# Optimization experiments

Hardware: AMD Instinct MI355X
Metric: run time of the kernel (lower is better)

Reference implementation:

```python
import jax, jax.numpy as jnp
import numpy as np
from jax import lax


def _l2n(t, eps=1e-12):
    n = jnp.sqrt(jnp.sum(t * t, axis=-1, keepdims=True))
    return t / jnp.maximum(n, eps)


def _ln(t, w, b, eps=1e-5):
    mu = jnp.mean(t, -1, keepdims=True)
    var = jnp.var(t, -1, keepdims=True)
    return (t - mu) / jnp.sqrt(var + eps) * w + b


def _unfold3(x):
    # nn.Unfold(kernel_size=3, padding=1, stride=1): [B,C,H,W] -> [B,C,9,H*W]
    B, C, H, W = x.shape
    xp = jnp.pad(x, ((0, 0), (0, 0), (1, 1), (1, 1)))
    pat = jnp.stack([xp[:, :, i:i + H, j:j + W] for i in range(3) for j in range(3)], axis=2)
    return pat.reshape(B, C, 9, H * W)


def _forward(x, norm1_w, norm1_b, q_w, q_b, kv_w, kv_b, temperature, query_embedding,
             learnable_tokens, learnable_bias, sr_w, sr_b, pln_w, pln_b, proj_w, proj_b,
             norm2_w, norm2_b, fc1_w, fc1_b, dw_w, dw_b, fc2_w, fc2_b):
    B, C, H, W = x.shape
    nh = temperature.shape[0]
    d = C // nh
    N = H * W
    K = 9  # local_len = window_size**2
    # norm1 (WithBias LayerNorm over channel dim, channels-last)
    y = _ln(x.reshape(B, C, N).transpose(0, 2, 1), norm1_w, norm1_b)  # [B,N,C]
    # ---- AggregatedAttention ----
    q = (y @ q_w.T + q_b).reshape(B, N, nh, d).transpose(0, 2, 1, 3)  # [B,h,N,d]
    qn = _l2n(q)
    qs = (qn + query_embedding) * jax.nn.softplus(temperature)
    kv = y @ kv_w.T + kv_b  # [B,N,2C]
    k_loc = _l2n(kv[..., :C].reshape(B, N, nh, d)).reshape(B, N, C)
    kvl = jnp.concatenate([k_loc, kv[..., C:]], -1).transpose(0, 2, 1).reshape(B, 2 * C, H, W)
    pat = _unfold3(kvl).reshape(B, 2 * nh, d, K, N).transpose(0, 1, 4, 2, 3)  # [B,2h,N,d,K]
    k_l, v_l = pat[:, :nh], pat[:, nh:]
    attn_local = jnp.einsum('bhnd,bhndk->bhnk', qs, k_l)  # [B,h,N,K]
    # pooled branch; sr_ratio=1 so adaptive_avg_pool2d is identity
    y4 = y.transpose(0, 2, 1).reshape(B, C, H, W)
    xp = jax.nn.gelu(jnp.einsum('oc,bchw->bohw', sr_w, y4) + sr_b[:, None, None], approximate=False)
    xp = _ln(xp.reshape(B, C, N).transpose(0, 2, 1), pln_w, pln_b)  # [B,pool_len,C]
    kvp = (xp @ kv_w.T + kv_b).reshape(B, N, 2 * nh, d).transpose(0, 2, 1, 3)
    k_p = _l2n(kvp[:, :nh])
    v_p = kvp[:, nh:]
    attn_pool = jnp.einsum('bhnd,bhmd->bhnm', qs, k_p)  # [B,h,N,pool_len]
    attn = jax.nn.softmax(jnp.concatenate([attn_local, attn_pool], -1), axis=-1)
    a_l, a_p = attn[..., :K], attn[..., K:]
    w_l = jnp.einsum('bhnd,hdk->bhnk', qn, learnable_tokens) + learnable_bias + a_l
    x_local = jnp.einsum('bhnk,bhndk->bhnd', w_l, v_l)
    x_pool = jnp.einsum('bhnm,bhmd->bhnd', a_p, v_p)
    xo = (x_local + x_pool).transpose(0, 2, 1, 3).reshape(B, N, C)
    # proj then raw torch-style reshape [B,N,C] -> [B,C,H,W] (memory reinterpretation)
    xo = (xo @ proj_w.T + proj_b).reshape(B, C, H, W)
    x = x + xo
    # ---- ConvolutionalGLU MLP ----
    hf = dw_b.shape[0]
    y2 = _ln(x.reshape(B, C, N).transpose(0, 2, 1), norm2_w, norm2_b).transpose(0, 2, 1).reshape(B, C, H, W)
    f1 = jnp.einsum('oc,bchw->bohw', fc1_w, y2) + fc1_b[:, None, None]
    a, v = f1[:, :hf], f1[:, hf:]
    dw = lax.conv_general_dilated(a, dw_w, (1, 1), ((1, 1), (1, 1)),
                                  feature_group_count=hf,
                                  dimension_numbers=('NCHW', 'OIHW', 'NCHW')) + dw_b[:, None, None]
    g = jax.nn.gelu(dw, approximate=False) * v
    out = jnp.einsum('oc,bchw->bohw', fc2_w, g) + fc2_b[:, None, None]
    return x + out


def setup_inputs() -> dict:
    key = jax.random.key(0)
    B, C, H, W = 2, 128, 56, 56
    nh, d, K = 4, 32, 9
    hf = int(2 * int(C * 4.0) / 3)  # 341
    ks = iter(jax.random.split(key, 16))
    rn = lambda shape, s=0.02: jax.random.normal(next(ks), shape, jnp.float32) * s
    return {
        'x': jax.random.normal(next(ks), (B, C, H, W), jnp.float32),
        'norm1_w': jnp.ones((C,), jnp.float32), 'norm1_b': jnp.zeros((C,), jnp.float32),
        'q_w': rn((C, C)), 'q_b': jnp.zeros((C,), jnp.float32),
        'kv_w': rn((2 * C, C)), 'kv_b': jnp.zeros((2 * C,), jnp.float32),
        'temperature': jnp.full((nh, 1, 1), float(np.log(np.exp(1.0 / 0.24) - 1.0)), jnp.float32),
        'query_embedding': rn((nh, 1, d)),
        'learnable_tokens': rn((nh, d, K)),
        'learnable_bias': jnp.zeros((nh, 1, K), jnp.float32),
        'sr_w': rn((C, C)), 'sr_b': jnp.zeros((C,), jnp.float32),
        'pln_w': jnp.ones((C,), jnp.float32), 'pln_b': jnp.zeros((C,), jnp.float32),
        'proj_w': rn((C, C)), 'proj_b': jnp.zeros((C,), jnp.float32),
        'norm2_w': jnp.ones((C,), jnp.float32), 'norm2_b': jnp.zeros((C,), jnp.float32),
        'fc1_w': rn((2 * hf, C)), 'fc1_b': jnp.zeros((2 * hf,), jnp.float32),
        'dw_w': rn((hf, 1, 3, 3)), 'dw_b': jnp.zeros((hf,), jnp.float32),
        'fc2_w': rn((C, hf)), 'fc2_b': jnp.zeros((C,), jnp.float32),
    }


def reference(x, norm1_w, norm1_b, q_w, q_b, kv_w, kv_b, temperature, query_embedding,
              learnable_tokens, learnable_bias, sr_w, sr_b, pln_w, pln_b, proj_w, proj_b,
              norm2_w, norm2_b, fc1_w, fc1_b, dw_w, dw_b, fc2_w, fc2_b):
    return _forward(x, norm1_w, norm1_b, q_w, q_b, kv_w, kv_b, temperature, query_embedding,
                    learnable_tokens, learnable_bias, sr_w, sr_b, pln_w, pln_b, proj_w, proj_b,
                    norm2_w, norm2_b, fc1_w, fc1_b, dw_w, dw_b, fc2_w, fc2_b)
```

## Files before the change

### kernel.cpp

```cpp
#include <hip/hip_runtime.h>
#include <hip/hip_bf16.h>

typedef __hip_bfloat16 bf16;
typedef short s8v __attribute__((ext_vector_type(8)));
typedef float f4v __attribute__((ext_vector_type(4)));

#define DEVI __device__ __forceinline__

DEVI float cvt(float x){ return x; }
DEVI float cvt(bf16 x){ return __bfloat162float(x); }

DEVI void stg(float* p, float v){ *p = v; }
DEVI void stg(bf16* p, float v){ *p = __float2bfloat16(v); }

DEVI float gelu_exact(float x){
  return 0.5f*x*(1.0f + erff(x*0.70710678118654752440f));
}

constexpr int B_ = 2, C_ = 128, H_ = 56, W_ = 56, N_ = 3136, NH_ = 4, D_ = 32, HF_ = 341;
constexpr int ROWS_ = B_*N_;
constexpr int KF2 = 352;
constexpr int GQ_ = NH_*B_*N_;
constexpr int FW = 512;
constexpr int KSP = 4;

template<typename TX, typename TY, bool PLANES>
__global__ __launch_bounds__(256)
void ln_kernel(const TX* __restrict__ x, long xstr, const float* __restrict__ w,
               const float* __restrict__ bia, TY* __restrict__ y)
{
  int gid = blockIdx.x*4 + (threadIdx.x>>6);
  int lane = threadIdx.x & 63;
  int b = gid / N_, n = gid % N_;
  float v0, v1;
  if (PLANES){
    v0 = cvt(x[((long)b*C_ + lane     )*N_ + n]);
    v1 = cvt(x[((long)b*C_ + lane + 64)*N_ + n]);
  } else {
    v0 = cvt(x[(long)gid*xstr + lane     ]);
    v1 = cvt(x[(long)gid*xstr + lane + 64]);
  }
  float s = v0+v1, ss = v0*v0 + v1*v1;
  #pragma unroll
  for (int o=32;o>0;o>>=1){ s += __shfl_xor(s,o); ss += __shfl_xor(ss,o); }
  float mu  = s*(1.0f/128.0f);
  float var = fmaxf(ss*(1.0f/128.0f) - mu*mu, 0.f);
  float inv = rsqrtf(var + 1e-5f);
  stg(&y[(long)gid*C_ + lane     ], (v0-mu)*inv*w[lane     ] + bia[lane     ]);
  stg(&y[(long)gid*C_ + lane + 64], (v1-mu)*inv*w[lane + 64] + bia[lane + 64]);
}

__global__ __launch_bounds__(256)
void convw_kernel(const float* __restrict__ q_w, const float* __restrict__ kv_w,
                  const float* __restrict__ sr_w, const float* __restrict__ proj_w,
                  const float* __restrict__ fc1_w, const float* __restrict__ fc2_w,
                  const float* __restrict__ q_b, const float* __restrict__ kv_b,
                  const float* __restrict__ sr_b,
                  bf16* __restrict__ out, float* __restrict__ bias_out)
{
  int t = blockIdx.x*256 + threadIdx.x;
  if (t >= 214272){
    int i = t - 214272;
    if (i < 512){
      float bv = (i < 128) ? q_b[i] : (i < 384) ? kv_b[i-128] : sr_b[i-384];
      bias_out[i] = bv;
    }
    return;
  }
  float v;
  if      (t <  16384) v = q_w[t];
  else if (t <  49152) v = kv_w[t-16384];
  else if (t <  65536) v = sr_w[t-49152];
  else if (t <  81920) v = proj_w[t-65536];
  else if (t < 169216) v = fc1_w[t-81920];
  else {
    int i = t - 169216; int m = i / KF2, kp = i % KF2;
    v = (kp < HF_) ? fc2_w[m*HF_ + kp] : 0.f;
  }
  out[t] = __float2bfloat16(v);
}

template<int KT, int MODE, typename TC>
__global__ __launch_bounds__(256)
void gemm_mfma(const bf16* __restrict__ A, const bf16* __restrict__ B,
               const float* __restrict__ bias, const float* __restrict__ res,
               TC* __restrict__ Cm, int M, int Nn,
               long sA, long sB, long sC, long sR)
{
  A  += (long)blockIdx.z * sA;
  B  += (long)blockIdx.z * sB;
  Cm += (long)blockIdx.z * sC;
  if (res) res += (long)blockIdx.z * sR;
  int lane = threadIdx.x & 63, w = threadIdx.x >> 6;
  int m = lane & 15, quad = lane >> 4;
  int n0 = blockIdx.x*64, m0 = blockIdx.y*64;
  int arow = m0 + w*16 + m;
  if (arow >= M) arow = M-1;
  const bf16* ap = A + (long)arow*KT + quad*8;
  const bf16* bp = B + (long)(n0 + m)*KT + quad*8;
  f4v acc[4];
  #pragma unroll
  for (int s=0;s<4;s++) acc[s] = (f4v){0.f,0.f,0.f,0.f};
  #pragma unroll
  for (int k0 = 0; k0 < KT; k0 += 32){
    s8v af = *(const s8v*)(ap + k0);
    #pragma unroll
    for (int s=0;s<4;s++){
      s8v bf = *(const s8v*)(bp + (long)s*16*KT + k0);
      acc[s] = __builtin_amdgcn_mfma_f32_16x16x32_bf16(af, bf, acc[s], 0, 0, 0);
    }
  }
  #pragma unroll
  for (int s=0;s<4;s++){
    int gn = n0 + s*16 + m;
    #pragma unroll
    for (int r=0;r<4;r++){
      int gm = m0 + w*16 + quad*4 + r;
      if (gm >= M) continue;
      float v = acc[s][r];
      if (MODE==1 || MODE==2 || MODE==4 || MODE==6) v += bias[gn];
      else                                          v += bias[gm];
      if (MODE==2) v = gelu_exact(v);
      if (MODE==6 && gn >= 384) v = gelu_exact(v);
      if (MODE==4 || MODE==5) v += res[(long)gm*Nn + gn];
      stg(&Cm[(long)gm*Nn + gn], v);
    }
  }
}

__global__ __launch_bounds__(256)
void post_q_kernel(const bf16* __restrict__ fused, const float* __restrict__ qe,
                   const float* __restrict__ temp, bf16* __restrict__ qs)
{
  int t = blockIdx.x*256 + threadIdx.x;
  int n = t % N_; int bh = t / N_; int h = bh & 3; int b = bh >> 2;
  float sp = log1pf(expf(temp[h]));
  const bf16* qr = fused + ((long)(b*N_ + n))*FW + h*D_;
  float v[32]; float ss = 0.f;
  #pragma unroll
  for (int d=0;d<32;d++){ v[d] = cvt(qr[d]); ss = fmaf(v[d], v[d], ss); }
  float inv = 1.f/fmaxf(sqrtf(ss), 1e-12f);
  bf16* qo = qs + ((long)bh*N_ + n)*D_;
  #pragma unroll
  for (int d=0;d<32;d++)
    stg(&qo[d], (v[d]*inv + qe[h*D_+d])*sp);
}

__global__ __launch_bounds__(256)
void post_kvp_kernel(const bf16* __restrict__ kvp_raw,
                     bf16* __restrict__ kp, bf16* __restrict__ vp)
{
  int t = blockIdx.x*256 + threadIdx.x;
  int n = t % N_; int bh = t / N_; int h = bh & 3; int b = bh >> 2;
  const bf16* kr = kvp_raw + ((long)(b*N_ + n))*(2*C_) + h*D_;
  float v[32]; float ss = 0.f;
  #pragma unroll
  for (int d=0;d<32;d++){ v[d] = cvt(kr[d]); ss = fmaf(v[d], v[d], ss); }
  float inv = 1.f/fmaxf(sqrtf(ss), 1e-12f);
  bf16* ko = kp + ((long)bh*N_ + n)*D_;
  #pragma unroll
  for (int d=0;d<32;d++) stg(&ko[d], v[d]*inv);
  #pragma unroll
  for (int d=0;d<32;d++) vp[((long)bh*D_ + d)*N_ + n] = kr[C_ + d];
}

__global__ __launch_bounds__(256)
void attn_part_kernel(const bf16* __restrict__ qs_, const bf16* __restrict__ kp_,
                      const bf16* __restrict__ vp_,
                      bf16* __restrict__ Op, float* __restrict__ Lp)
{
  int bh = blockIdx.y;
  int z  = blockIdx.z;
  int lane = threadIdx.x & 63;
  int w    = threadIdx.x >> 6;
  int m    = lane & 15, quad = lane >> 4;
  int base = blockIdx.x*256 + w*16;
  __shared__ float sm[4][2304];
  bf16*  Pl   = (bf16*)sm[w];
  float* Olds = sm[w];

  s8v af[4]; bool hasQ[4];
  #pragma unroll
  for (int ch=0; ch<4; ch++){
    int qq = base + ch*64;
    hasQ[ch] = (qq < N_);
    af[ch] = *(const s8v*)(qs_ + ((long)bh*N_ + (hasQ[ch] ? qq : base) + m)*D_ + quad*8);
  }
  const bf16* kpb = kp_ + (long)bh*N_*D_;
  const bf16* vpb = vp_ + (long)bh*D_*N_;
  f4v o0[4], o1[4];
  float l[4][4];
  #pragma unroll
  for (int ch=0; ch<4; ch++){
    o0[ch] = (f4v){0.f,0.f,0.f,0.f}; o1[ch] = (f4v){0.f,0.f,0.f,0.f};
    #pragma unroll
    for (int r=0;r<4;r++) l[ch][r] = 0.f;
  }

  int tlo = z*768, thi = (z==3) ? N_ : tlo + 768;
  for (int t0 = tlo; t0 < thi; t0 += 64){
    s8v kf[4], vf[4];
    #pragma unroll
    for (int s=0;s<4;s++)
      kf[s] = *(const s8v*)(kpb + (long)(t0 + s*16 + m)*D_ + quad*8);
    vf[0] = *(const s8v*)(vpb + (long)(m     )*N_ + t0      + quad*8);
    vf[1] = *(const s8v*)(vpb + (long)(16 + m)*N_ + t0      + quad*8);
    vf[2] = *(const s8v*)(vpb + (long)(m     )*N_ + t0 + 32 + quad*8);
    vf[3] = *(const s8v*)(vpb + (long)(16 + m)*N_ + t0 + 32 + quad*8);
    #pragma unroll
    for (int s = 0; s < 4; s++){
      #pragma unroll
      for (int ch=0; ch<4; ch++){
        f4v c = {0.f,0.f,0.f,0.f};
        c = __builtin_amdgcn_mfma_f32_16x16x32_bf16(af[ch], kf[s], c, 0, 0, 0);
        #pragma unroll
        for (int r=0;r<4;r++){
          float e = __expf(c[r] - 8.f);
          l[ch][r] += e;
          Pl[ch*1152 + (quad*4+r)*72 + s*16 + m] = __float2bfloat16(e);
        }
      }
    }
    #pragma unroll
    for (int c2=0;c2<2;c2++){
      #pragma unroll
      for (int ch=0; ch<4; ch++){
        s8v pa = *(const s8v*)(Pl + ch*1152 + m*72 + c2*32 + quad*8);
        o0[ch] = __builtin_amdgcn_mfma_f32_16x16x32_bf16(pa, vf[c2*2  ], o0[ch], 0, 0, 0);
        o1[ch] = __builtin_amdgcn_mfma_f32_16x16x32_bf16(pa, vf[c2*2+1], o1[ch], 0, 0, 0);
      }
    }
  }
  #pragma unroll
  for (int ch=0; ch<4; ch++){
    if (!hasQ[ch]) continue;
    float lr[4] = {l[ch][0], l[ch][1], l[ch][2], l[ch][3]};
    #pragma unroll
    for (int off=1; off<16; off<<=1)
      #pragma unroll
      for (int r=0;r<4;r++) lr[r] += __shfl_xor(lr[r], off);
    #pragma unroll
    for (int r=0;r<4;r++){
      Olds[(quad*4+r)*36 + m     ] = o0[ch][r];
      Olds[(quad*4+r)*36 + 16 + m] = o1[ch][r];
    }
    if (m == 0){
      #pragma unroll
      for (int r=0;r<4;r++) Olds[576 + quad*4 + r] = lr[r];
    }
    long gq = (long)bh*N_ + base + ch*64 + m;
    f4v ov0 = *(const f4v*)(Olds + m*36 + quad*8);
    f4v ov1 = *(const f4v*)(Olds + m*36 + quad*8 + 4);
    bf16 o8[8];
    #pragma unroll
    for (int j=0;j<4;j++){ o8[j] = __float2bfloat16(ov0[j]); o8[4+j] = __float2bfloat16(ov1[j]); }
    *(s8v*)(Op + ((long)z*GQ_ + gq)*32 + quad*8) = *(const s8v*)o8;
    if (quad == 0) Lp[(long)z*GQ_ + gq] = Olds[576 + m];
  }
}

__global__ __launch_bounds__(256)
void attn_combine_kernel(const bf16* __restrict__ Op, const float* __restrict__ Lp,
                         const bf16* __restrict__ qs_, const bf16* __restrict__ fused,
                         const float* __restrict__ qe, const float* __restrict__ temp,
                         const float* __restrict__ tokens, const float* __restrict__ tbias,
                         bf16* __restrict__ xo)
{
  int gq = blockIdx.x*256 + threadIdx.x;
  int n = gq % N_; int bh = gq / N_; int h = bh & 3; int b = bh >> 2;
  float L = 0.f;
  float out[32];
  #pragma unroll
  for (int d=0;d<32;d++) out[d] = 0.f;
  #pragma unroll
  for (int z=0; z<KSP; z++){
    L += Lp[(long)z*GQ_ + gq];
    const bf16* oz = Op + ((long)z*GQ_ + gq)*32;
    #pragma unroll
    for (int d=0;d<32;d++) out[d] += cvt(oz[d]);
  }
  const bf16* qrow = qs_ + (long)gq*D_;
  float q[32];
  #pragma unroll
  for (int d=0;d<32;d++) q[d] = cvt(qrow[d]);
  int hy = n / W_, wx = n % W_;
  const bf16* kvb = fused + (long)b*N_*FW + 128 + h*D_;
  float sl[9];
  #pragma unroll
  for (int k=0;k<9;k++){
    int di = k/3-1, dj = k%3-1;
    int yy = hy+di, xx = wx+dj;
    float s = 0.f;
    if (yy>=0 && yy<H_ && xx>=0 && xx<W_){
      long nn2 = (long)(yy*W_+xx)*FW;
      float dot = 0.f, ss = 0.f;
      #pragma unroll
      for (int d=0;d<32;d++){
        float kk = cvt(kvb[nn2 + d]);
        dot = fmaf(q[d], kk, dot);
        ss  = fmaf(kk, kk, ss);
      }
      s = dot / fmaxf(sqrtf(ss), 1e-12f);
    }
    sl[k] = s;
  }
  #pragma unroll
  for (int k=0;k<9;k++) L += __expf(sl[k] - 8.f);
  float invL = 1.f/L;
  #pragma unroll
  for (int d=0;d<32;d++) out[d] *= invL;
  float sp = log1pf(expf(temp[h]));
  float invsp = 1.f/sp;
  float qn[32];
  #pragma unroll
  for (int d=0;d<32;d++) qn[d] = q[d]*invsp - qe[h*D_+d];
  #pragma unroll
  for (int k=0;k<9;k++){
    float tok = 0.f;
    #pragma unroll
    for (int d=0;d<32;d++) tok = fmaf(qn[d], tokens[(h*D_+d)*9+k], tok);
    float wl = tok + tbias[h*9+k] + __expf(sl[k] - 8.f)*invL;
    int di = k/3-1, dj = k%3-1;
    int yy = hy+di, xx = wx+dj;
    if (yy>=0 && yy<H_ && xx>=0 && xx<W_){
      long nn2 = (long)(yy*W_+xx)*FW;
      #pragma unroll
      for (int d=0;d<32;d++) out[d] = fmaf(wl, cvt(kvb[nn2 + 128 + d]), out[d]);
    }
  }
  bf16* op = xo + ((long)(b*N_ + n))*C_ + h*D_;
  #pragma unroll
  for (int d=0;d<32;d++) stg(&op[d], out[d]);
}

__global__ __launch_bounds__(256)
void dwconv_kernel(const bf16* __restrict__ f1, const float* __restrict__ dww,
                   const float* __restrict__ dwb, bf16* __restrict__ g)
{
  int t = blockIdx.x*256 + threadIdx.x;
  if (t >= B_*N_*44) return;
  int b = t / (N_*44); int r = t - b*(N_*44);
  int n = r % N_, cg = r / N_;
  f1 += (long)b*2*HF_*N_;
  g  += (long)b*N_*KF2;
  int c0 = cg*8;
  int hy = n / W_, wx = n % W_;
  bf16 o8[8];
  #pragma unroll
  for (int j=0;j<8;j++){
    int c = c0 + j;
    float val = 0.f;
    if (c < HF_){
      const bf16* ap = f1 + (long)c*N_;
      float s = dwb[c];
      #pragma unroll
      for (int di=-1; di<=1; di++)
        #pragma unroll
        for (int dj=-1; dj<=1; dj++){
          int yy = hy+di, xx = wx+dj;
          if (yy>=0 && yy<H_ && xx>=0 && xx<W_)
            s = fmaf(dww[c*9 + (di+1)*3 + (dj+1)], cvt(ap[yy*W_+xx]), s);
        }
      val = gelu_exact(s) * cvt(f1[(long)(HF_+c)*N_ + n]);
    }
    o8[j] = __float2bfloat16(val);
  }
  *(s8v*)(g + (long)n*KF2 + c0) = *(const s8v*)o8;
}

extern "C" void kernel_launch(void* const* d_in, const int* in_sizes, int n_in,
                              void* d_out, int out_size, void* d_ws, size_t ws_size,
                              hipStream_t stream)
{
  (void)in_sizes; (void)n_in; (void)out_size; (void)ws_size;
  const float* x_in      = (const float*)d_in[0];
  const float* norm1_w   = (const float*)d_in[1];
  const float* norm1_b   = (const float*)d_in[2];
  const float* q_w       = (const float*)d_in[3];
  const float* q_b       = (const float*)d_in[4];
  const float* kv_w      = (const float*)d_in[5];
  const float* kv_b      = (const float*)d_in[6];
  const float* temp      = (const float*)d_in[7];
  const float* qe        = (const float*)d_in[8];
  const float* tokens    = (const float*)d_in[9];
  const float* tbias     = (const float*)d_in[10];
  const float* sr_w      = (const float*)d_in[11];
  const float* sr_b      = (const float*)d_in[12];
  const float* pln_w     = (const float*)d_in[13];
  const float* pln_b     = (const float*)d_in[14];
  const float* proj_w    = (const float*)d_in[15];
  const float* proj_b    = (const float*)d_in[16];
  const float* norm2_w   = (const float*)d_in[17];
  const float* norm2_b   = (const float*)d_in[18];
  const float* fc1_w     = (const float*)d_in[19];
  const float* fc1_b     = (const float*)d_in[20];
  const float* dw_w      = (const float*)d_in[21];
  const float* dw_b      = (const float*)d_in[22];
  const float* fc2_w     = (const float*)d_in[23];
  const float* fc2_b     = (const float*)d_in[24];

  char* w8 = (char*)d_ws;
  bf16*  fused   = (bf16*)(w8 + 0);
  float* x2      = (float*)(w8 + 0);
  bf16*  y2      = (bf16*)(w8 + 3211264);
  bf16*  f1b     = (bf16*)(w8 + 4816896);
  bf16*  qs      = (bf16*)(w8 + 6422528);
  bf16*  xp      = (bf16*)(w8 + 8028160);
  bf16*  k_p     = (bf16*)(w8 + 8028160);
  bf16*  v_p     = (bf16*)(w8 + 9633792);
  bf16*  kvp_raw = (bf16*)(w8 + 11239424);
  bf16*  Opart   = (bf16*)(w8 + 11239424);
  bf16*  g_rows  = (bf16*)(w8 + 17661952);
  bf16*  wbase   = (bf16*)(w8 + 22077440);
  float* fbias   = (float*)(w8 + 22505984);
  bf16*  y       = f1b;
  bf16*  xo      = (bf16*)d_out;
  float* Lpart   = (float*)((char*)d_out + 1605632);
  bf16*  proj_wb = wbase + 65536;
  bf16*  fc1_wb  = wbase + 81920;
  bf16*  fc2_wb  = wbase + 169216;

  convw_kernel<<<(214784+255)/256, 256, 0, stream>>>(
      q_w, kv_w, sr_w, proj_w, fc1_w, fc2_w, q_b, kv_b, sr_b, wbase, fbias);
  ln_kernel<float, bf16, true><<<ROWS_/4, 256, 0, stream>>>(x_in, 0, norm1_w, norm1_b, y);
  gemm_mfma<128, 6, bf16><<<dim3(8,98), 256, 0, stream>>>(
      y, wbase, fbias, nullptr, fused, ROWS_, FW, 0,0,0,0);
  post_q_kernel<<<98, 256, 0, stream>>>(fused, qe, temp, qs);
  ln_kernel<bf16, bf16, false><<<ROWS_/4, 256, 0, stream>>>(fused + 384, FW, pln_w, pln_b, xp);
  gemm_mfma<128, 1, bf16><<<dim3(4,98), 256, 0, stream>>>(
      xp, wbase + 16384, kv_b, nullptr, kvp_raw, ROWS_, 256, 0,0,0,0);
  post_kvp_kernel<<<98, 256, 0, stream>>>(kvp_raw, k_p, v_p);
  attn_part_kernel<<<dim3(13,8,KSP), 256, 0, stream>>>(qs, k_p, v_p, Opart, Lpart);
  attn_combine_kernel<<<GQ_/256, 256, 0, stream>>>(Opart, Lpart, qs, fused,
                                                   qe, temp, tokens, tbias, xo);
  gemm_mfma<128, 4, float><<<dim3(2,98), 256, 0, stream>>>(
      xo, proj_wb, proj_b, x_in, x2, ROWS_, 128, 0,0,0,0);
  ln_kernel<float, bf16, true><<<ROWS_/4, 256, 0, stream>>>(x2, 0, norm2_w, norm2_b, y2);
  gemm_mfma<128, 3, bf16><<<dim3(49,11,B_), 256, 0, stream>>>(
      fc1_wb, y2, fc1_b, nullptr, f1b, 2*HF_, N_,
      0, (long)N_*C_, (long)2*HF_*N_, 0);
  dwconv_kernel<<<(B_*N_*44+255)/256, 256, 0, stream>>>(f1b, dw_w, dw_b, g_rows);
  gemm_mfma<KF2, 5, float><<<dim3(49,2,B_), 256, 0, stream>>>(
      fc2_wb, g_rows, fc2_b, x2, (float*)d_out, C_, N_,
      0, (long)N_*KF2, (long)C_*N_, (long)C_*N_);
}
```

Before: 272.3 us.

## Fuse q/kv-pool L2-norm epilogues into GEMMs and double attention split-K

Moves the q normalization, query-embedding and softplus scaling into the fused QKV GEMM epilogue, and the pooled-K normalization plus V transpose into the kv-pool GEMM epilogue. Row norms are computed with cross-lane shuffles, so the post_q and post_kvp kernels and their round trip through the intermediate buffers are no longer needed. Separately, the attention key range is split into 8 chunks instead of 4 to expose more parallel blocks. The extra splits cost more partial-result traffic in the combine step, and the workspace buffers are re-laid out to fit the larger Opart.

```diff
diff --git a/kernel.cpp b/kernel.cpp
--- a/kernel.cpp
+++ b/kernel.cpp
@@ -3,6 +3,7 @@
 
 typedef __hip_bfloat16 bf16;
 typedef short s8v __attribute__((ext_vector_type(8)));
+typedef short s4v __attribute__((ext_vector_type(4)));
 typedef float f4v __attribute__((ext_vector_type(4)));
 
 #define DEVI __device__ __forceinline__
@@ -22,7 +23,7 @@
 constexpr int KF2 = 352;
 constexpr int GQ_ = NH_*B_*N_;
 constexpr int FW = 512;
-constexpr int KSP = 4;
+constexpr int KSP = 8;
 
 template<typename TX, typename TY, bool PLANES>
 __global__ __launch_bounds__(256)
@@ -85,7 +86,9 @@
 void gemm_mfma(const bf16* __restrict__ A, const bf16* __restrict__ B,
                const float* __restrict__ bias, const float* __restrict__ res,
                TC* __restrict__ Cm, int M, int Nn,
-               long sA, long sB, long sC, long sR)
+               long sA, long sB, long sC, long sR,
+               const float* __restrict__ qe, const float* __restrict__ temp,
+               bf16* __restrict__ aux0, bf16* __restrict__ aux1)
 {
   A  += (long)blockIdx.z * sA;
   B  += (long)blockIdx.z * sB;
@@ -110,6 +113,51 @@
       acc[s] = __builtin_amdgcn_mfma_f32_16x16x32_bf16(af, bf, acc[s], 0, 0, 0);
     }
   }
+  if ((MODE==6 || MODE==7) && blockIdx.x < 2){
+    int hA = blockIdx.x*2, hB = hA+1;
+    float spA = 0.f, spB = 0.f;
+    if (MODE==6){ spA = log1pf(expf(temp[hA])); spB = log1pf(expf(temp[hB])); }
+    #pragma unroll
+    for (int r=0;r<4;r++){
+      float v4[4];
+      #pragma unroll
+      for (int s=0;s<4;s++) v4[s] = acc[s][r] + bias[n0 + s*16 + m];
+      float ssA = v4[0]*v4[0] + v4[1]*v4[1];
+      float ssB = v4[2]*v4[2] + v4[3]*v4[3];
+      #pragma unroll
+      for (int off=1; off<16; off<<=1){
+        ssA += __shfl_xor(ssA, off);
+        ssB += __shfl_xor(ssB, off);
+      }
+      float invA = 1.f/fmaxf(sqrtf(ssA), 1e-12f);
+      float invB = 1.f/fmaxf(sqrtf(ssB), 1e-12f);
+      int gm = m0 + w*16 + quad*4 + r;
+      int b = gm / N_, n = gm % N_;
+      #pragma unroll
+      for (int s=0;s<4;s++){
+        int h = (s<2) ? hA : hB;
+        int d = (s&1)*16 + m;
+        float v = v4[s] * ((s<2) ? invA : invB);
+        if (MODE==6) v = (v + qe[h*D_ + d]) * ((s<2) ? spA : spB);
+        aux0[((long)(b*NH_+h)*N_ + n)*D_ + d] = __float2bfloat16(v);
+      }
+    }
+    return;
+  }
+  if (MODE==7){
+    int gm0 = m0 + w*16 + quad*4;
+    int b = gm0 / N_, nb = gm0 % N_;
+    #pragma unroll
+    for (int s=0;s<4;s++){
+      int h = (blockIdx.x-2)*2 + (s>>1);
+      int d = (s&1)*16 + m;
+      bf16 p4[4];
+      #pragma unroll
+      for (int r=0;r<4;r++) p4[r] = __float2bfloat16(acc[s][r] + bias[n0 + s*16 + m]);
+      *(s4v*)(aux1 + ((long)(b*NH_+h)*D_ + d)*N_ + nb) = *(const s4v*)p4;
+    }
+    return;
+  }
   #pragma unroll
   for (int s=0;s<4;s++){
     int gn = n0 + s*16 + m;
@@ -118,50 +166,13 @@
       int gm = m0 + w*16 + quad*4 + r;
       if (gm >= M) continue;
       float v = acc[s][r];
-      if (MODE==1 || MODE==2 || MODE==4 || MODE==6) v += bias[gn];
-      else                                          v += bias[gm];
-      if (MODE==2) v = gelu_exact(v);
+      if (MODE==1 || MODE==4 || MODE==6) v += bias[gn];
+      else                               v += bias[gm];
       if (MODE==6 && gn >= 384) v = gelu_exact(v);
       if (MODE==4 || MODE==5) v += res[(long)gm*Nn + gn];
       stg(&Cm[(long)gm*Nn + gn], v);
     }
   }
-}
-
-__global__ __launch_bounds__(256)
-void post_q_kernel(const bf16* __restrict__ fused, const float* __restrict__ qe,
-                   const float* __restrict__ temp, bf16* __restrict__ qs)
-{
-  int t = blockIdx.x*256 + threadIdx.x;
-  int n = t % N_; int bh = t / N_; int h = bh & 3; int b = bh >> 2;
-  float sp = log1pf(expf(temp[h]));
-  const bf16* qr = fused + ((long)(b*N_ + n))*FW + h*D_;
-  float v[32]; float ss = 0.f;
-  #pragma unroll
-  for (int d=0;d<32;d++){ v[d] = cvt(qr[d]); ss = fmaf(v[d], v[d], ss); }
-  float inv = 1.f/fmaxf(sqrtf(ss), 1e-12f);
-  bf16* qo = qs + ((long)bh*N_ + n)*D_;
-  #pragma unroll
-  for (int d=0;d<32;d++)
-    stg(&qo[d], (v[d]*inv + qe[h*D_+d])*sp);
-}
-
-__global__ __launch_bounds__(256)
-void post_kvp_kernel(const bf16* __restrict__ kvp_raw,
-                     bf16* __restrict__ kp, bf16* __restrict__ vp)
-{
-  int t = blockIdx.x*256 + threadIdx.x;
-  int n = t % N_; int bh = t / N_; int h = bh & 3; int b = bh >> 2;
-  const bf16* kr = kvp_raw + ((long)(b*N_ + n))*(2*C_) + h*D_;
-  float v[32]; float ss = 0.f;
-  #pragma unroll
-  for (int d=0;d<32;d++){ v[d] = cvt(kr[d]); ss = fmaf(v[d], v[d], ss); }
-  float inv = 1.f/fmaxf(sqrtf(ss), 1e-12f);
-  bf16* ko = kp + ((long)bh*N_ + n)*D_;
-  #pragma unroll
-  for (int d=0;d<32;d++) stg(&ko[d], v[d]*inv);
-  #pragma unroll
-  for (int d=0;d<32;d++) vp[((long)bh*D_ + d)*N_ + n] = kr[C_ + d];
 }
 
 __global__ __launch_bounds__(256)
@@ -197,7 +208,7 @@
     for (int r=0;r<4;r++) l[ch][r] = 0.f;
   }
 
-  int tlo = z*768, thi = (z==3) ? N_ : tlo + 768;
+  int tlo = z*384, thi = (z==KSP-1) ? N_ : tlo + 384;
   for (int t0 = tlo; t0 < thi; t0 += 64){
     s8v kf[4], vf[4];
     #pragma unroll
@@ -406,13 +417,12 @@
   bf16*  f1b     = (bf16*)(w8 + 4816896);
   bf16*  qs      = (bf16*)(w8 + 6422528);
   bf16*  xp      = (bf16*)(w8 + 8028160);
-  bf16*  k_p     = (bf16*)(w8 + 8028160);
-  bf16*  v_p     = (bf16*)(w8 + 9633792);
-  bf16*  kvp_raw = (bf16*)(w8 + 11239424);
-  bf16*  Opart   = (bf16*)(w8 + 11239424);
-  bf16*  g_rows  = (bf16*)(w8 + 17661952);
-  bf16*  wbase   = (bf16*)(w8 + 22077440);
-  float* fbias   = (float*)(w8 + 22505984);
+  bf16*  k_p     = (bf16*)(w8 + 9633792);
+  bf16*  v_p     = (bf16*)(w8 + 11239424);
+  bf16*  Opart   = (bf16*)(w8 + 13045056);
+  bf16*  g_rows  = (bf16*)(w8 + 25890112);
+  bf16*  wbase   = (bf16*)(w8 + 30305600);
+  float* fbias   = (float*)(w8 + 30734144);
   bf16*  y       = f1b;
   bf16*  xo      = (bf16*)d_out;
   float* Lpart   = (float*)((char*)d_out + 1605632);
@@ -424,23 +434,22 @@
       q_w, kv_w, sr_w, proj_w, fc1_w, fc2_w, q_b, kv_b, sr_b, wbase, fbias);
   ln_kernel<float, bf16, true><<<ROWS_/4, 256, 0, stream>>>(x_in, 0, norm1_w, norm1_b, y);
   gemm_mfma<128, 6, bf16><<<dim3(8,98), 256, 0, stream>>>(
-      y, wbase, fbias, nullptr, fused, ROWS_, FW, 0,0,0,0);
-  post_q_kernel<<<98, 256, 0, stream>>>(fused, qe, temp, qs);
+      y, wbase, fbias, nullptr, fused, ROWS_, FW, 0,0,0,0, qe, temp, qs, nullptr);
   ln_kernel<bf16, bf16, false><<<ROWS_/4, 256, 0, stream>>>(fused + 384, FW, pln_w, pln_b, xp);
-  gemm_mfma<128, 1, bf16><<<dim3(4,98), 256, 0, stream>>>(
-      xp, wbase + 16384, kv_b, nullptr, kvp_raw, ROWS_, 256, 0,0,0,0);
-  post_kvp_kernel<<<98, 256, 0, stream>>>(kvp_raw, k_p, v_p);
+  gemm_mfma<128, 7, bf16><<<dim3(4,98), 256, 0, stream>>>(
+      xp, wbase + 16384, kv_b, nullptr, (bf16*)nullptr, ROWS_, 256, 0,0,0,0,
+      nullptr, nullptr, k_p, v_p);
   attn_part_kernel<<<dim3(13,8,KSP), 256, 0, stream>>>(qs, k_p, v_p, Opart, Lpart);
   attn_combine_kernel<<<GQ_/256, 256, 0, stream>>>(Opart, Lpart, qs, fused,
                                                    qe, temp, tokens, tbias, xo);
   gemm_mfma<128, 4, float><<<dim3(2,98), 256, 0, stream>>>(
-      xo, proj_wb, proj_b, x_in, x2, ROWS_, 128, 0,0,0,0);
+      xo, proj_wb, proj_b, x_in, x2, ROWS_, 128, 0,0,0,0, nullptr, nullptr, nullptr, nullptr);
   ln_kernel<float, bf16, true><<<ROWS_/4, 256, 0, stream>>>(x2, 0, norm2_w, norm2_b, y2);
   gemm_mfma<128, 3, bf16><<<dim3(49,11,B_), 256, 0, stream>>>(
       fc1_wb, y2, fc1_b, nullptr, f1b, 2*HF_, N_,
-      0, (long)N_*C_, (long)2*HF_*N_, 0);
+      0, (long)N_*C_, (long)2*HF_*N_, 0, nullptr, nullptr, nullptr, nullptr);
   dwconv_kernel<<<(B_*N_*44+255)/256, 256, 0, stream>>>(f1b, dw_w, dw_b, g_rows);
   gemm_mfma<KF2, 5, float><<<dim3(49,2,B_), 256, 0, stream>>>(
       fc2_wb, g_rows, fc2_b, x2, (float*)d_out, C_, N_,
-      0, (long)N_*KF2, (long)C_*N_, (long)C_*N_);
-}
+      0, (long)N_*KF2, (long)C_*N_, (long)C_*N_, nullptr, nullptr, nullptr, nullptr);
+}
```

Measured after the change: 269.0 us. About the same (-1.2%).
